# Performance work log

Hardware: AMD Instinct MI355X
Metric: run time of the kernel (lower is better)

## Reference

```python
import jax, jax.numpy as jnp
import numpy as np
from jax import lax

N = 2048
B = 64
T = 128
INPUT_DIM = 4
OUTPUT_DIM = 2
N_SENS = 256
N_OUT = 128


def setup_inputs() -> dict:
    key = jax.random.key(0)
    ks = jax.random.split(key, 6)
    inputs = jax.random.normal(ks[0], (B, T, INPUT_DIM), dtype=jnp.float32)
    # scale recurrent weights so repeated relu(h@W) does not blow up
    W_rec = jax.random.normal(ks[1], (N, N), dtype=jnp.float32) * (0.9 / np.sqrt(N))
    scale_in = 1.0 / np.sqrt(INPUT_DIM)
    scale_out = 1.0 / np.sqrt(N_OUT)
    W_in = jax.random.uniform(ks[2], (N_SENS, INPUT_DIM), dtype=jnp.float32,
                              minval=-scale_in, maxval=scale_in)
    b_in = jnp.zeros((N_SENS,), dtype=jnp.float32)
    W_out = jax.random.uniform(ks[3], (OUTPUT_DIM, N_OUT), dtype=jnp.float32,
                               minval=-scale_out, maxval=scale_out)
    b_out = jnp.zeros((OUTPUT_DIM,), dtype=jnp.float32)
    sensory_indices = jax.random.permutation(ks[4], N)[:N_SENS].astype(jnp.int64)
    output_indices = jax.random.permutation(ks[5], N)[:N_OUT].astype(jnp.int64)
    return {"inputs": inputs, "W_rec": W_rec, "W_in": W_in, "b_in": b_in,
            "W_out": W_out, "b_out": b_out,
            "sensory_indices": sensory_indices, "output_indices": output_indices,
            "K": 4}


def reference(inputs, W_rec, W_in, b_in, W_out, b_out,
              sensory_indices, output_indices, K):
    # inputs: [B, T, I]; h: [B, N]
    rec_t = W_rec.T  # h @ W_rec.T as in torch code
    batch = inputs.shape[0]
    h0 = jnp.zeros((batch, W_rec.shape[0]), dtype=inputs.dtype)

    def micro(h, _):
        return jax.nn.relu(h @ rec_t), None

    def timestep(h, x_t):  # x_t: [B, I]
        injection = x_t @ W_in.T + b_in               # [B, n_sens]
        next_h = (h @ rec_t).at[:, sensory_indices].add(injection)
        h = jax.nn.relu(next_h)                       # microstep 0
        h, _ = lax.scan(micro, h, None, length=K - 1) # remaining microsteps
        readout = h[:, output_indices] @ W_out.T + b_out  # [B, OUTPUT_DIM]
        return h, readout

    _, outs = lax.scan(timestep, h0, jnp.swapaxes(inputs, 0, 1))  # [T, B, O]
    return jnp.swapaxes(outs, 0, 1)  # [B, T, O]
```

## Files before the change

kernel.cpp:

```cpp
#include <hip/hip_runtime.h>


#define N_DIM   2048
#define B_DIM   64
#define T_DIM   128
#define NSENS   256
#define NOUT    128
#define NSTEP   512

#define NWG     256
#define THREADS 512
#define CW      32
#define RING    3
#define SLOT_F16 (B_DIM * N_DIM)
#define SP_S    20
#define SP_HALF (256 * SP_S)
#define LDS_W_F16 (CW * N_DIM)
#define SMEM_MAIN (LDS_W_F16 * 2 + 2 * SP_HALF * 2)

typedef _Float16 f16x8 __attribute__((ext_vector_type(8)));
typedef _Float16 f16x4 __attribute__((ext_vector_type(4)));
typedef float    f32x4 __attribute__((ext_vector_type(4)));
typedef unsigned long long u64;
typedef unsigned short u16;

#define SIGN_M32 0x80008000u
#define SIGN_M64 0x8000800080008000ULL

union V16 { uint4 q; u64 u[2]; };


__global__ void k_init(uint4* __restrict__ ring, int* __restrict__ inv_sens,
                       int* __restrict__ inv_out, u64* __restrict__ flags) {
    const int i = blockIdx.x * blockDim.x + threadIdx.x;
    const int slot = i / (SLOT_F16 / 8);
    if (slot < RING) {
        const unsigned pat = (slot == 0 || (slot & 1)) ? SIGN_M32 : 0u;
        ring[i] = make_uint4(pat, pat, pat, pat);
    }
    if (i < N_DIM) { inv_sens[i] = -1; inv_out[i] = -1; }
    if (i < 64) flags[i] = 0ull;
}

__global__ void k_inv_scatter(int* inv_sens, int* inv_out,
                              const int* sidx, const int* oidx) {
    int i = threadIdx.x;
    if (i < NSENS) inv_sens[sidx[i]] = i;
    if (i < NOUT)  inv_out[oidx[i]] = i;
}


__global__ __launch_bounds__(THREADS, 2)
void rnn_main(const float* __restrict__ W_rec, const float* __restrict__ inputs,
              const float* __restrict__ W_in, const float* __restrict__ b_in,
              const int* __restrict__ inv_sens, const int* __restrict__ inv_out,
              _Float16* __restrict__ ring, _Float16* __restrict__ hc,
              u16* __restrict__ flags )
{
    extern __shared__ _Float16 smem[];
    _Float16* w_hi = smem;
    _Float16* sp   = smem + LDS_W_F16;

    const int tid   = threadIdx.x;
    const int wg    = blockIdx.x;
    const int pl    = wg & 3;
    const int cg    = wg >> 2;
    const int jbase = cg * CW;

    const int lane = tid & 63;
    const int wv   = tid >> 6;
    const int lrow = lane & 15;
    const int quad = lane >> 4;
    (void)flags;

    f16x8 blo[8][2];
#pragma unroll
    for (int nt = 0; nt < 2; ++nt) {
        const float* wr = W_rec + (size_t)(jbase + nt * 16 + lrow) * N_DIM
                        + wv * 256 + quad * 8;
#pragma unroll
        for (int ks = 0; ks < 8; ++ks) {
            const float4 wa = ((const float4*)(wr + ks * 32))[0];
            const float4 wb = ((const float4*)(wr + ks * 32))[1];
            const float w8[8] = {wa.x, wa.y, wa.z, wa.w, wb.x, wb.y, wb.z, wb.w};
            f16x8 hi8;
#pragma unroll
            for (int e = 0; e < 8; ++e) {
                const _Float16 hi = (_Float16)w8[e];
                hi8[e] = hi;
                blo[ks][nt][e] = (_Float16)((w8[e] - (float)hi) * 4096.0f);
            }
            *(f16x8*)(w_hi + ((((wv * 8 + ks) * 2 + nt)) << 9) + lane * 8) = hi8;
        }
    }

    const int eo    = wv * 32 + (lane & 31);
    const int ebl   = eo >> 4;
    const int ejp   = eo & 15;
    const int ehalf = lane >> 5;
    const int ep_b  = pl * 16 + ebl;
    const int ej    = jbase + ejp * 2;
    const int ep_sA = inv_sens[ej], ep_sB = inv_sens[ej + 1];
    const int ep_uA = inv_out[ej],  ep_uB = inv_out[ej + 1];
    const int ep_off = ((pl * 64 + cg) << 9)
                     + ((((ej >> 3) & 3) * 16 + ebl) << 3) + (ej & 7);

    float4 wA = {0.f, 0.f, 0.f, 0.f}, wB = {0.f, 0.f, 0.f, 0.f};
    float  bA = 0.f, bB = 0.f;
    if (ep_sA >= 0) { wA = *(const float4*)(W_in + (ep_sA << 2)); bA = b_in[ep_sA]; }
    if (ep_sB >= 0) { wB = *(const float4*)(W_in + (ep_sB << 2)); bB = b_in[ep_sB]; }
    __syncthreads();

    int slot_r = 0, slot_w = 1;

    for (int step = 0; step < NSTEP; ++step) {
        const int t = step >> 2, micro = step & 3;
        const bool expSet = (step & 1) == 0;
        const _Float16* __restrict__ hcur = ring + (size_t)slot_r * SLOT_F16;
        _Float16* __restrict__       hnxt = ring + (size_t)slot_w * SLOT_F16;

        float4 x = {0.f, 0.f, 0.f, 0.f};
        if (micro == 0) x = *(const float4*)(inputs + ((ep_b * T_DIM + t) << 2));

        const _Float16* hb = hcur + ((pl * 64 + wv * 8) << 9) + lane * 8;
        V16 a[8];
        asm volatile(
            "global_load_dwordx4 %0, %8, off sc1\n\t"
            "global_load_dwordx4 %1, %9, off sc1\n\t"
            "global_load_dwordx4 %2, %10, off sc1\n\t"
            "global_load_dwordx4 %3, %11, off sc1\n\t"
            "global_load_dwordx4 %4, %12, off sc1\n\t"
            "global_load_dwordx4 %5, %13, off sc1\n\t"
            "global_load_dwordx4 %6, %14, off sc1\n\t"
            "global_load_dwordx4 %7, %15, off sc1"
            : "=v"(a[0].q), "=v"(a[1].q), "=v"(a[2].q), "=v"(a[3].q),
              "=v"(a[4].q), "=v"(a[5].q), "=v"(a[6].q), "=v"(a[7].q)
            : "v"(hb),        "v"(hb + 512),  "v"(hb + 1024), "v"(hb + 1536),
              "v"(hb + 2048), "v"(hb + 2560), "v"(hb + 3072), "v"(hb + 3584)
            : "memory");

        f16x8 bh[8][2];
#pragma unroll
        for (int ks = 0; ks < 8; ++ks)
#pragma unroll
            for (int nt = 0; nt < 2; ++nt)
                bh[ks][nt] = *(const f16x8*)(w_hi + (((wv * 8 + ks) * 2 + nt) << 9) + lane * 8);

        f32x4 acch[2], accl[2];
#pragma unroll
        for (int nt = 0; nt < 2; ++nt) {
            acch[nt] = (f32x4){0.f, 0.f, 0.f, 0.f};
            accl[nt] = (f32x4){0.f, 0.f, 0.f, 0.f};
        }

        asm volatile("s_waitcnt vmcnt(0)" ::: "memory");
        __builtin_amdgcn_sched_barrier(0);

        unsigned live = 0xFFu;
        while (live) {
#pragma unroll
            for (int f = 0; f < 8; ++f) if (live & (1u << f)) {
                const u64 band = a[f].u[0] & a[f].u[1];
                const u64 bor  = a[f].u[0] | a[f].u[1];
                const bool ok = expSet ? ((band & SIGN_M64) == SIGN_M64)
                                       : ((bor  & SIGN_M64) == 0);
                if (__all((int)ok)) {
                    union { u64 u[2]; f16x8 v; } c;
                    c.u[0] = expSet ? (a[f].u[0] ^ SIGN_M64) : a[f].u[0];
                    c.u[1] = expSet ? (a[f].u[1] ^ SIGN_M64) : a[f].u[1];
                    const f16x8 Af = c.v;
                    acch[0] = __builtin_amdgcn_mfma_f32_16x16x32_f16(Af, bh[f][0], acch[0], 0, 0, 0);
                    accl[0] = __builtin_amdgcn_mfma_f32_16x16x32_f16(Af, blo[f][0], accl[0], 0, 0, 0);
                    acch[1] = __builtin_amdgcn_mfma_f32_16x16x32_f16(Af, bh[f][1], acch[1], 0, 0, 0);
                    accl[1] = __builtin_amdgcn_mfma_f32_16x16x32_f16(Af, blo[f][1], accl[1], 0, 0, 0);
                    live &= ~(1u << f);
                }
            }
            if (live) {
                __builtin_amdgcn_s_sleep(1);
#pragma unroll
                for (int f = 0; f < 8; ++f) if (live & (1u << f))
                    asm volatile("global_load_dwordx4 %0, %1, off sc1"
                                 : "=v"(a[f].q) : "v"(hb + f * 512) : "memory");
                asm volatile("s_waitcnt vmcnt(0)" ::: "memory");
                __builtin_amdgcn_sched_barrier(0);
            }
        }

        _Float16* sph = sp + (step & 1) * SP_HALF;
#pragma unroll
        for (int nt = 0; nt < 2; ++nt) {
            f16x4 pv;
#pragma unroll
            for (int r = 0; r < 4; ++r)
                pv[r] = (_Float16)(acch[nt][r] + accl[nt][r] * 2.44140625e-4f);
            *(f16x4*)(sph + (wv * 32 + nt * 16 + lrow) * SP_S + quad * 4) = pv;
        }
        __syncthreads();

        {
            float vA = 0.f, vB = 0.f;
#pragma unroll
            for (int s = 0; s < 4; ++s) {
                const int s8 = ehalf * 4 + s;
                vA += (float)sph[(s8 * 32 + ejp * 2    ) * SP_S + ebl];
                vB += (float)sph[(s8 * 32 + ejp * 2 + 1) * SP_S + ebl];
            }
            vA += __shfl_xor(vA, 32, 64);
            vB += __shfl_xor(vB, 32, 64);
            if (lane < 32) {
                if (micro == 0) {
                    vA += bA + x.x * wA.x + x.y * wA.y + x.z * wA.z + x.w * wA.w;
                    vB += bB + x.x * wB.x + x.y * wB.y + x.z * wB.z + x.w * wB.w;
                }
                union { _Float16 h[2]; unsigned u; } pk;
                pk.h[0] = (_Float16)fmaxf(vA, 0.0f);
                pk.h[1] = (_Float16)fmaxf(vB, 0.0f);
                const unsigned pr = pk.u | ((step & 1) ? SIGN_M32 : 0u);
                __hip_atomic_store((unsigned*)(hnxt + ep_off), pr,
                                   __ATOMIC_RELAXED, __HIP_MEMORY_SCOPE_AGENT);
                if (micro == 3) {
                    if (ep_uA >= 0) hc[(t * NOUT + ep_uA) * B_DIM + ep_b] = pk.h[0];
                    if (ep_uB >= 0) hc[(t * NOUT + ep_uB) * B_DIM + ep_b] = pk.h[1];
                }
            }
        }
        __syncthreads();

        slot_r = (slot_r + 1 == RING) ? 0 : slot_r + 1;
        slot_w = (slot_w + 1 == RING) ? 0 : slot_w + 1;
    }
}


__global__ __launch_bounds__(128)
void k_readout(float* __restrict__ out, const _Float16* __restrict__ hc,
               const float* __restrict__ W_out, const float* __restrict__ b_out) {
    __shared__ _Float16 sh[NOUT * B_DIM];
    const int t = blockIdx.x, tid = threadIdx.x;
    const unsigned int* src = (const unsigned int*)(hc + (size_t)t * NOUT * B_DIM);
    for (int i = tid; i < NOUT * B_DIM / 2; i += 128)
        ((unsigned int*)sh)[i] = src[i];
    __syncthreads();
    const int o = tid >> 6, b = tid & 63;
    float acc = b_out[o];
#pragma unroll 8
    for (int u = 0; u < NOUT; ++u)
        acc += (float)sh[u * B_DIM + b] * W_out[o * NOUT + u];
    out[(b * T_DIM + t) * 2 + o] = acc;
}


extern "C" void kernel_launch(void* const* d_in, const int* in_sizes, int n_in,
                              void* d_out, int out_size, void* d_ws, size_t ws_size,
                              hipStream_t stream) {
    const float* inputs = (const float*)d_in[0];
    const float* W_rec  = (const float*)d_in[1];
    const float* W_in   = (const float*)d_in[2];
    const float* b_in   = (const float*)d_in[3];
    const float* W_out  = (const float*)d_in[4];
    const float* b_out  = (const float*)d_in[5];
    const int*   sidx   = (const int*)d_in[6];
    const int*   oidx   = (const int*)d_in[7];

    char* ws = (char*)d_ws;
    _Float16* ring     = (_Float16*)ws;
    _Float16* hc       = (_Float16*)(ws + 786432);
    int*      inv_sens = (int*)(ws + 786432 + 2097152);
    int*      inv_out  = inv_sens + N_DIM;
    u16*      flags    = (u16*)(inv_out + N_DIM);

    k_init<<<192, 256, 0, stream>>>((uint4*)ring, inv_sens, inv_out, (u64*)flags);
    k_inv_scatter<<<1, 256, 0, stream>>>(inv_sens, inv_out, sidx, oidx);

    (void)hipFuncSetAttribute((const void*)rnn_main,
                              hipFuncAttributeMaxDynamicSharedMemorySize, SMEM_MAIN);

    rnn_main<<<NWG, THREADS, SMEM_MAIN, stream>>>(
        W_rec, inputs, W_in, b_in, inv_sens, inv_out, ring, hc, flags);

    k_readout<<<T_DIM, 128, 0, stream>>>((float*)d_out, hc, W_out, b_out);
}
```

Baseline: 1.309 ms.

## Use XCC-local cache policy for polling loads from same-XCC producers

Each workgroup publishes its XCC id to a flags array and then discovers which producer workgroups share its XCC. Polling loads of h fragments from those producers use sc0 (device-coherent but possibly served from the shared L2) instead of sc1 system-scope loads. After 16 failed polling rounds the code falls back to sc1 loads to avoid stale-cache livelock. This adds a startup spin on the flags and relies on the XCC-to-L2 coherence assumptions holding.

```diff
diff --git a/kernel.cpp b/kernel.cpp
--- a/kernel.cpp
+++ b/kernel.cpp
@@ -71,7 +71,13 @@
     const int wv   = tid >> 6;
     const int lrow = lane & 15;
     const int quad = lane >> 4;
-    (void)flags;
+
+    unsigned myxcc;
+    asm volatile("s_getreg_b32 %0, hwreg(HW_REG_XCC_ID)" : "=s"(myxcc));
+    myxcc &= 7;
+    if (tid == 0)
+        __hip_atomic_store(&flags[wg], (u16)(myxcc + 1),
+                           __ATOMIC_RELAXED, __HIP_MEMORY_SCOPE_AGENT);
 
     f16x8 blo[8][2];
 #pragma unroll
@@ -109,6 +115,20 @@
     float  bA = 0.f, bB = 0.f;
     if (ep_sA >= 0) { wA = *(const float4*)(W_in + (ep_sA << 2)); bA = b_in[ep_sA]; }
     if (ep_sB >= 0) { wB = *(const float4*)(W_in + (ep_sB << 2)); bB = b_in[ep_sB]; }
+
+    unsigned locmask = 0;
+#pragma unroll
+    for (int f = 0; f < 8; ++f) {
+        const int wgp = (wv * 8 + f) * 4 + pl;
+        unsigned v;
+        while (true) {
+            v = __hip_atomic_load(&flags[wgp], __ATOMIC_RELAXED,
+                                  __HIP_MEMORY_SCOPE_AGENT);
+            if (v) break;
+            __builtin_amdgcn_s_sleep(8);
+        }
+        if (v - 1 == myxcc) locmask |= (1u << f);
+    }
     __syncthreads();
 
     int slot_r = 0, slot_w = 1;
@@ -124,20 +144,15 @@
 
         const _Float16* hb = hcur + ((pl * 64 + wv * 8) << 9) + lane * 8;
         V16 a[8];
-        asm volatile(
-            "global_load_dwordx4 %0, %8, off sc1\n\t"
-            "global_load_dwordx4 %1, %9, off sc1\n\t"
-            "global_load_dwordx4 %2, %10, off sc1\n\t"
-            "global_load_dwordx4 %3, %11, off sc1\n\t"
-            "global_load_dwordx4 %4, %12, off sc1\n\t"
-            "global_load_dwordx4 %5, %13, off sc1\n\t"
-            "global_load_dwordx4 %6, %14, off sc1\n\t"
-            "global_load_dwordx4 %7, %15, off sc1"
-            : "=v"(a[0].q), "=v"(a[1].q), "=v"(a[2].q), "=v"(a[3].q),
-              "=v"(a[4].q), "=v"(a[5].q), "=v"(a[6].q), "=v"(a[7].q)
-            : "v"(hb),        "v"(hb + 512),  "v"(hb + 1024), "v"(hb + 1536),
-              "v"(hb + 2048), "v"(hb + 2560), "v"(hb + 3072), "v"(hb + 3584)
-            : "memory");
+#pragma unroll
+        for (int f = 0; f < 8; ++f) {
+            if (locmask & (1u << f))
+                asm volatile("global_load_dwordx4 %0, %1, off sc0"
+                             : "=v"(a[f].q) : "v"(hb + f * 512) : "memory");
+            else
+                asm volatile("global_load_dwordx4 %0, %1, off sc1"
+                             : "=v"(a[f].q) : "v"(hb + f * 512) : "memory");
+        }
 
         f16x8 bh[8][2];
 #pragma unroll
@@ -157,6 +172,7 @@
         __builtin_amdgcn_sched_barrier(0);
 
         unsigned live = 0xFFu;
+        int rounds = 0;
         while (live) {
 #pragma unroll
             for (int f = 0; f < 8; ++f) if (live & (1u << f)) {
@@ -178,10 +194,16 @@
             }
             if (live) {
                 __builtin_amdgcn_s_sleep(1);
-#pragma unroll
-                for (int f = 0; f < 8; ++f) if (live & (1u << f))
-                    asm volatile("global_load_dwordx4 %0, %1, off sc1"
-                                 : "=v"(a[f].q) : "v"(hb + f * 512) : "memory");
+                const bool esc = (++rounds >= 16);
+#pragma unroll
+                for (int f = 0; f < 8; ++f) if (live & (1u << f)) {
+                    if (!esc && (locmask & (1u << f)))
+                        asm volatile("global_load_dwordx4 %0, %1, off sc0"
+                                     : "=v"(a[f].q) : "v"(hb + f * 512) : "memory");
+                    else
+                        asm volatile("global_load_dwordx4 %0, %1, off sc1"
+                                     : "=v"(a[f].q) : "v"(hb + f * 512) : "memory");
+                }
                 asm volatile("s_waitcnt vmcnt(0)" ::: "memory");
                 __builtin_amdgcn_sched_barrier(0);
             }
```

Measured after the change: 1.996 ms. 52.5% more time.
